# Performance work log

Hardware: AMD Instinct MI355X
Metric: run time of the kernel (lower is better)

Reference implementation:

```python
import jax, jax.numpy as jnp
from jax import lax
import numpy as np

H = 2048
LX = 32
LY = 32


def setup_inputs() -> dict:
    key = jax.random.key(0)
    ks = jax.random.split(key, 9)
    N = LX * LY
    s = 1.0 / np.sqrt(H).astype(np.float32)
    inp = {
        "x": jax.random.normal(ks[0], (N,), jnp.float32),
        # embed: Dense(1 -> H)
        "We": jax.random.normal(ks[1], (1, H), jnp.float32),
        "be": jnp.zeros((H,), jnp.float32),
        # GRUCell input gates (with bias)
        "Wir": jax.random.normal(ks[2], (H, H), jnp.float32) * s,
        "bir": jnp.zeros((H,), jnp.float32),
        "Wiz": jax.random.normal(ks[3], (H, H), jnp.float32) * s,
        "biz": jnp.zeros((H,), jnp.float32),
        "Win": jax.random.normal(ks[4], (H, H), jnp.float32) * s,
        "bin_": jnp.zeros((H,), jnp.float32),
        # GRUCell recurrent gates (hr/hz bias-free, hn with bias, as in flax)
        "Whr": jax.random.normal(ks[5], (H, H), jnp.float32) * s,
        "Whz": jax.random.normal(ks[6], (H, H), jnp.float32) * s,
        "Whn": jax.random.normal(ks[7], (H, H), jnp.float32) * s,
        "bhn": jnp.zeros((H,), jnp.float32),
        "Lx": LX,
        "Ly": LY,
    }
    return inp


def snake_order(Lx: int, Ly: int):
    idx = np.arange(Lx * Ly).reshape(Ly, Lx)
    idx[1::2] = idx[1::2, ::-1]  # reverse odd rows -> snake pattern
    return jnp.asarray(idx.reshape(-1))


def reference(x, We, be, Wir, bir, Wiz, biz, Win, bin_, Whr, Whz, Whn, bhn, Lx, Ly):
    order = snake_order(Lx, Ly)                      # (N,) visit order
    # embed each scalar site value: Dense(1->H), vectorized over all sites
    xe = x[order][:, None] * We[0][None, :] + be     # (N, H)
    # precompute input-gate projections for all steps (same math, batched)
    a_r = xe @ Wir + bir                             # (N, H)
    a_z = xe @ Wiz + biz
    a_n = xe @ Win + bin_
    h0 = jnp.zeros((Whr.shape[0],), xe.dtype)

    def step(h, g):
        ar, az, an = g
        r = jax.nn.sigmoid(ar + h @ Whr)
        z = jax.nn.sigmoid(az + h @ Whz)
        n = jnp.tanh(an + r * (h @ Whn + bhn))
        h_new = (1.0 - z) * n + z * h
        return h_new, None

    h, _ = lax.scan(step, h0, (a_r, a_z, a_n))
    return h
```

## Files before the change

### kernel.cpp

```cpp
#include <hip/hip_runtime.h>

#define HDIM 2048
#define TSTEPS 1024
#define NBLK 256
#define NTHR 512
#define CPB 8
#define TAGM 0x3FFu
#define NREP 8
#define RSTRIDE 2112u

typedef unsigned long long ull;

__device__ __forceinline__ int snake_src(int t) {
    int y = t >> 5, p = t & 31;
    return (y & 1) ? (y * 32 + 31 - p) : t;
}
__device__ __forceinline__ float sigmoid_f(float v) {
    return __builtin_amdgcn_rcpf(1.f + __expf(-v));
}
__device__ __forceinline__ float tanh_f(float v) {
    return 1.f - 2.f * __builtin_amdgcn_rcpf(__expf(2.f * v) + 1.f);
}

__global__ __launch_bounds__(NTHR, 2) void gru_all(
    const float* __restrict__ x,
    const float* __restrict__ We,  const float* __restrict__ be,
    const float* __restrict__ Wir, const float* __restrict__ bir,
    const float* __restrict__ Wiz, const float* __restrict__ biz,
    const float* __restrict__ Win, const float* __restrict__ bin_,
    const float* __restrict__ Whr, const float* __restrict__ Whz,
    const float* __restrict__ Whn, const float* __restrict__ bhn,
    float* __restrict__ out, unsigned* __restrict__ u0, unsigned* __restrict__ u1)
{
    const int tid  = threadIdx.x;
    const int blk  = blockIdx.x;
    const int c    = tid & 7;
    const int r    = tid >> 3;
    const int col  = blk * CPB + c;
    const int row0 = r * 32;
    const int lane = tid & 63, wv = tid >> 6;

    __shared__ __align__(16) float lds_h[2304];
    __shared__ float red[8][6][8];
    __shared__ float sX[TSTEPS];

    for (int i = tid; i < TSTEPS; i += NTHR) sX[i] = x[snake_src(i)];

    float wr[32], wz[32], wn[32];
#pragma unroll
    for (int k = 0; k < 32; ++k) {
        size_t off = (size_t)(row0 + k) * HDIM + col;
        wr[k] = Whr[off];
        wz[k] = Whz[off];
        wn[k] = Whn[off];
    }

    float eR=0,eZ=0,eN=0,bRa=0,bZa=0,bNa=0;
#pragma unroll 8
    for (int k = 0; k < 32; ++k) {
        int row = row0 + k;
        size_t off = (size_t)row * HDIM + col;
        float we = We[row], bb = be[row];
        float w0 = Wir[off], w1 = Wiz[off], w2 = Win[off];
        eR  = fmaf(we, w0, eR);  bRa = fmaf(bb, w0, bRa);
        eZ  = fmaf(we, w1, eZ);  bZa = fmaf(bb, w1, bZa);
        eN  = fmaf(we, w2, eN);  bNa = fmaf(bb, w2, bNa);
    }
#pragma unroll
    for (int m = 8; m < 64; m <<= 1) {
        eR  += __shfl_xor(eR,  m, 64); eZ  += __shfl_xor(eZ,  m, 64);
        eN  += __shfl_xor(eN,  m, 64); bRa += __shfl_xor(bRa, m, 64);
        bZa += __shfl_xor(bZa, m, 64); bNa += __shfl_xor(bNa, m, 64);
    }
    if (lane < 8) {
        red[wv][0][lane]=eR;  red[wv][1][lane]=eZ;  red[wv][2][lane]=eN;
        red[wv][3][lane]=bRa; red[wv][4][lane]=bZa; red[wv][5][lane]=bNa;
    }
    __syncthreads();

    float vrc=0,vzc=0,vnc=0,crc=0,czc=0,cnc=0,bhc=0;
    float aR=0, aZ=0, aN=0;
    unsigned pk1 = 0;
    if (tid < 8) {
#pragma unroll
        for (int w = 0; w < 8; ++w) {
            vrc += red[w][0][tid]; vzc += red[w][1][tid]; vnc += red[w][2][tid];
            crc += red[w][3][tid]; czc += red[w][4][tid]; cnc += red[w][5][tid];
        }
        crc += bir[col]; czc += biz[col]; cnc += bin_[col];
        bhc = bhn[col];

        float x0 = sX[0];
        float ar = fmaf(x0, vrc, crc);
        float az = fmaf(x0, vzc, czc);
        float an = fmaf(x0, vnc, cnc);
        float rg = sigmoid_f(ar), zg = sigmoid_f(az);
        float ng = tanh_f(fmaf(rg, bhc, an));
        float h1 = (1.f - zg) * ng;
        pk1 = ((__float_as_uint(h1) + 512u) & ~TAGM) | 1u;

        float x1 = sX[1];
        aR = fmaf(x1, vrc, crc);
        aZ = fmaf(x1, vzc, czc);
        aN = fmaf(x1, vnc, cnc);
    }
    if (wv == 0) {
        unsigned pkb = __shfl(pk1, lane & 7, 64);
        __hip_atomic_store(&u1[(unsigned)(lane >> 3) * RSTRIDE + (unsigned)blk * 8u + (unsigned)(lane & 7)],
                           pkb, __ATOMIC_RELAXED, __HIP_MEMORY_SCOPE_AGENT);
    }

    const int sbase = tid * 4;
    const int lwb   = sbase + ((sbase >> 6) << 2);
    const int lrb   = row0  + ((row0  >> 6) << 2);
    const int pcol  = col   + ((col   >> 6) << 2);
    const ull  M2   = 0x000003FF000003FFull;
    const size_t repoff = (size_t)(blk & 7) * (RSTRIDE / 2);

    for (int t = 1; t < TSTEPS; ++t) {
        const unsigned* pin  = (t & 1) ? u1 : u0;
        unsigned*       pout = (t & 1) ? u0 : u1;
        const unsigned  tg   = (unsigned)t & TAGM;
        const ull       tg2  = ((ull)tg << 32) | (ull)tg;

        const ull* pp = (const ull*)pin + repoff + 2 * tid;
        ull v0 = __hip_atomic_load(&pp[0], __ATOMIC_RELAXED, __HIP_MEMORY_SCOPE_AGENT);
        ull v1 = __hip_atomic_load(&pp[1], __ATOMIC_RELAXED, __HIP_MEMORY_SCOPE_AGENT);
        while (((v0 ^ tg2) | (v1 ^ tg2)) & M2) {
            __builtin_amdgcn_s_sleep(1);
            v0 = __hip_atomic_load(&pp[0], __ATOMIC_RELAXED, __HIP_MEMORY_SCOPE_AGENT);
            v1 = __hip_atomic_load(&pp[1], __ATOMIC_RELAXED, __HIP_MEMORY_SCOPE_AGENT);
        }
        float4 hq = make_float4(__uint_as_float((unsigned)v0         & ~TAGM),
                                __uint_as_float((unsigned)(v0 >> 32) & ~TAGM),
                                __uint_as_float((unsigned)v1         & ~TAGM),
                                __uint_as_float((unsigned)(v1 >> 32) & ~TAGM));
        *(float4*)&lds_h[lwb] = hq;
        __syncthreads();

        float hold = 0.f;
        if (wv == 0) hold = lds_h[pcol];

        float a0 = 0.f, a1 = 0.f, a2 = 0.f;
#pragma unroll
        for (int k = 0; k < 32; ++k) {
            float hv = lds_h[lrb + k];
            a0 = fmaf(hv, wr[k], a0);
            a1 = fmaf(hv, wz[k], a1);
            a2 = fmaf(hv, wn[k], a2);
        }
#pragma unroll
        for (int m = 8; m < 64; m <<= 1) {
            a0 += __shfl_xor(a0, m, 64);
            a1 += __shfl_xor(a1, m, 64);
            a2 += __shfl_xor(a2, m, 64);
        }
        if (lane < 8) { red[wv][0][lane]=a0; red[wv][1][lane]=a1; red[wv][2][lane]=a2; }
        __syncthreads();

        if (wv == 0) {
            float hnew = 0.f; unsigned pk = 0;
            if (lane < 8) {
                float Sr=0, Sz=0, Sn=0;
#pragma unroll
                for (int w = 0; w < 8; ++w) {
                    Sr += red[w][0][lane]; Sz += red[w][1][lane]; Sn += red[w][2][lane];
                }
                float ar = aR + Sr;
                float az = aZ + Sz;
                float rg = sigmoid_f(ar), zg = sigmoid_f(az);
                float ng = tanh_f(aN + rg * (Sn + bhc));
                hnew = (1.f - zg) * ng + zg * hold;
                pk = ((__float_as_uint(hnew) + 512u) & ~TAGM)
                   | ((unsigned)(t + 1) & TAGM);
            }
            if (t == TSTEPS - 1) {
                if (lane < 8) out[col] = hnew;
            } else {
                unsigned pkb = __shfl(pk, lane & 7, 64);
                __hip_atomic_store(&pout[(unsigned)(lane >> 3) * RSTRIDE + (unsigned)blk * 8u + (unsigned)(lane & 7)],
                                   pkb, __ATOMIC_RELAXED, __HIP_MEMORY_SCOPE_AGENT);
                if (lane < 8) {
                    float xn = sX[t + 1];
                    aR = fmaf(xn, vrc, crc);
                    aZ = fmaf(xn, vzc, czc);
                    aN = fmaf(xn, vnc, cnc);
                }
            }
        }
        __syncthreads();
    }
}

extern "C" void kernel_launch(void* const* d_in, const int* in_sizes, int n_in,
                              void* d_out, int out_size, void* d_ws, size_t ws_size,
                              hipStream_t stream) {
    const float* x    = (const float*)d_in[0];
    const float* We   = (const float*)d_in[1];
    const float* be   = (const float*)d_in[2];
    const float* Wir  = (const float*)d_in[3];
    const float* bir  = (const float*)d_in[4];
    const float* Wiz  = (const float*)d_in[5];
    const float* biz  = (const float*)d_in[6];
    const float* Win  = (const float*)d_in[7];
    const float* bin_ = (const float*)d_in[8];
    const float* Whr  = (const float*)d_in[9];
    const float* Whz  = (const float*)d_in[10];
    const float* Whn  = (const float*)d_in[11];
    const float* bhn  = (const float*)d_in[12];

    unsigned* u0 = (unsigned*)d_ws;
    unsigned* u1 = u0 + NREP * RSTRIDE;

    gru_all<<<NBLK, NTHR, 0, stream>>>(x, We, be, Wir, bir, Wiz, biz, Win, bin_,
                                       Whr, Whz, Whn, bhn,
                                       (float*)d_out, u0, u1);
}
```

Baseline: 2.257 ms.

## Broadcast h via ds_swizzle, LDS atomic reduction, and 16 replicas with 64-bit stores

Each thread now keeps the four h values it polled in registers and shares them within 8-lane groups using ds_swizzle broadcasts. This removes the LDS staging buffer and one __syncthreads per step. The per-wave partial sums are combined with LDS atomicAdd into accumulators pre-seeded with the input-gate terms, replacing the separate reduction array. The h-state is published to 16 replicas using packed 64-bit stores, which spreads polling contention across more copies. Risks are atomicAdd ordering nondeterminism, more global store traffic, and launch_bounds dropping to one block per CU.

Result: slower. 2.468 ms (+9.3%).

```diff
diff --git a/kernel.cpp b/kernel.cpp
--- a/kernel.cpp
+++ b/kernel.cpp
@@ -6,7 +6,7 @@
 #define NTHR 512
 #define CPB 8
 #define TAGM 0x3FFu
-#define NREP 8
+#define NREP 16
 #define RSTRIDE 2112u
 
 typedef unsigned long long ull;
@@ -21,8 +21,13 @@
 __device__ __forceinline__ float tanh_f(float v) {
     return 1.f - 2.f * __builtin_amdgcn_rcpf(__expf(2.f * v) + 1.f);
 }
-
-__global__ __launch_bounds__(NTHR, 2) void gru_all(
+template<int G>
+__device__ __forceinline__ float bcast8(float v) {
+    return __uint_as_float((unsigned)__builtin_amdgcn_ds_swizzle(
+        (int)__float_as_uint(v), (G << 5) | 0x18));
+}
+
+__global__ __launch_bounds__(NTHR, 1) void gru_all(
     const float* __restrict__ x,
     const float* __restrict__ We,  const float* __restrict__ be,
     const float* __restrict__ Wir, const float* __restrict__ bir,
@@ -40,9 +45,10 @@
     const int row0 = r * 32;
     const int lane = tid & 63, wv = tid >> 6;
 
-    __shared__ __align__(16) float lds_h[2304];
     __shared__ float red[8][6][8];
     __shared__ float sX[TSTEPS];
+    __shared__ float sAcc[3][8];
+    __shared__ float sHold[8];
 
     for (int i = tid; i < TSTEPS; i += NTHR) sX[i] = x[snake_src(i)];
 
@@ -79,7 +85,7 @@
     __syncthreads();
 
     float vrc=0,vzc=0,vnc=0,crc=0,czc=0,cnc=0,bhc=0;
-    float aR=0, aZ=0, aN=0;
+    float aN=0;
     unsigned pk1 = 0;
     if (tid < 8) {
 #pragma unroll
@@ -100,22 +106,24 @@
         pk1 = ((__float_as_uint(h1) + 512u) & ~TAGM) | 1u;
 
         float x1 = sX[1];
-        aR = fmaf(x1, vrc, crc);
-        aZ = fmaf(x1, vzc, czc);
-        aN = fmaf(x1, vnc, cnc);
+        sAcc[0][tid] = fmaf(x1, vrc, crc);
+        sAcc[1][tid] = fmaf(x1, vzc, czc);
+        aN           = fmaf(x1, vnc, cnc);
+        sAcc[2][tid] = bhc;
     }
     if (wv == 0) {
-        unsigned pkb = __shfl(pk1, lane & 7, 64);
-        __hip_atomic_store(&u1[(unsigned)(lane >> 3) * RSTRIDE + (unsigned)blk * 8u + (unsigned)(lane & 7)],
-                           pkb, __ATOMIC_RELAXED, __HIP_MEMORY_SCOPE_AGENT);
-    }
-
-    const int sbase = tid * 4;
-    const int lwb   = sbase + ((sbase >> 6) << 2);
-    const int lrb   = row0  + ((row0  >> 6) << 2);
-    const int pcol  = col   + ((col   >> 6) << 2);
-    const ull  M2   = 0x000003FF000003FFull;
-    const size_t repoff = (size_t)(blk & 7) * (RSTRIDE / 2);
+        unsigned c0  = (lane & 3) * 2;
+        unsigned pkA = __shfl(pk1, (int)c0,     64);
+        unsigned pkB = __shfl(pk1, (int)c0 + 1, 64);
+        ull pkk = (ull)pkA | ((ull)pkB << 32);
+        ull* dst = (ull*)u1 + (ull)(lane >> 2) * (RSTRIDE / 2)
+                 + (ull)blk * 4 + (ull)(lane & 3);
+        __hip_atomic_store(dst, pkk, __ATOMIC_RELAXED, __HIP_MEMORY_SCOPE_AGENT);
+    }
+    __syncthreads();
+
+    const ull  M2     = 0x000003FF000003FFull;
+    const ull  repoff = (ull)(blk & 15) * (RSTRIDE / 2);
 
     for (int t = 1; t < TSTEPS; ++t) {
         const unsigned* pin  = (t & 1) ? u1 : u0;
@@ -131,45 +139,49 @@
             v0 = __hip_atomic_load(&pp[0], __ATOMIC_RELAXED, __HIP_MEMORY_SCOPE_AGENT);
             v1 = __hip_atomic_load(&pp[1], __ATOMIC_RELAXED, __HIP_MEMORY_SCOPE_AGENT);
         }
-        float4 hq = make_float4(__uint_as_float((unsigned)v0         & ~TAGM),
-                                __uint_as_float((unsigned)(v0 >> 32) & ~TAGM),
-                                __uint_as_float((unsigned)v1         & ~TAGM),
-                                __uint_as_float((unsigned)(v1 >> 32) & ~TAGM));
-        *(float4*)&lds_h[lwb] = hq;
-        __syncthreads();
-
-        float hold = 0.f;
-        if (wv == 0) hold = lds_h[pcol];
+        float hr0 = __uint_as_float((unsigned)v0         & ~TAGM);
+        float hr1 = __uint_as_float((unsigned)(v0 >> 32) & ~TAGM);
+        float hr2 = __uint_as_float((unsigned)v1         & ~TAGM);
+        float hr3 = __uint_as_float((unsigned)(v1 >> 32) & ~TAGM);
+
+        if ((tid >> 1) == blk) {
+            float* hs = &sHold[(tid & 1) * 4];
+            hs[0] = hr0; hs[1] = hr1; hs[2] = hr2; hs[3] = hr3;
+        }
 
         float a0 = 0.f, a1 = 0.f, a2 = 0.f;
-#pragma unroll
-        for (int k = 0; k < 32; ++k) {
-            float hv = lds_h[lrb + k];
-            a0 = fmaf(hv, wr[k], a0);
-            a1 = fmaf(hv, wz[k], a1);
-            a2 = fmaf(hv, wn[k], a2);
-        }
+#define GRP(G) { \
+        float h0 = bcast8<G>(hr0), h1 = bcast8<G>(hr1); \
+        float h2 = bcast8<G>(hr2), h3 = bcast8<G>(hr3); \
+        a0 = fmaf(h0, wr[4*G+0], a0); a1 = fmaf(h0, wz[4*G+0], a1); a2 = fmaf(h0, wn[4*G+0], a2); \
+        a0 = fmaf(h1, wr[4*G+1], a0); a1 = fmaf(h1, wz[4*G+1], a1); a2 = fmaf(h1, wn[4*G+1], a2); \
+        a0 = fmaf(h2, wr[4*G+2], a0); a1 = fmaf(h2, wz[4*G+2], a1); a2 = fmaf(h2, wn[4*G+2], a2); \
+        a0 = fmaf(h3, wr[4*G+3], a0); a1 = fmaf(h3, wz[4*G+3], a1); a2 = fmaf(h3, wn[4*G+3], a2); }
+        GRP(0) GRP(1) GRP(2) GRP(3) GRP(4) GRP(5) GRP(6) GRP(7)
+#undef GRP
+
 #pragma unroll
         for (int m = 8; m < 64; m <<= 1) {
             a0 += __shfl_xor(a0, m, 64);
             a1 += __shfl_xor(a1, m, 64);
             a2 += __shfl_xor(a2, m, 64);
         }
-        if (lane < 8) { red[wv][0][lane]=a0; red[wv][1][lane]=a1; red[wv][2][lane]=a2; }
+        if (lane < 8) {
+            atomicAdd(&sAcc[0][lane], a0);
+            atomicAdd(&sAcc[1][lane], a1);
+            atomicAdd(&sAcc[2][lane], a2);
+        }
         __syncthreads();
 
         if (wv == 0) {
             float hnew = 0.f; unsigned pk = 0;
             if (lane < 8) {
-                float Sr=0, Sz=0, Sn=0;
-#pragma unroll
-                for (int w = 0; w < 8; ++w) {
-                    Sr += red[w][0][lane]; Sz += red[w][1][lane]; Sn += red[w][2][lane];
-                }
-                float ar = aR + Sr;
-                float az = aZ + Sz;
-                float rg = sigmoid_f(ar), zg = sigmoid_f(az);
-                float ng = tanh_f(aN + rg * (Sn + bhc));
+                float Sr = sAcc[0][lane];
+                float Sz = sAcc[1][lane];
+                float Sn = sAcc[2][lane];
+                float hold = sHold[lane];
+                float rg = sigmoid_f(Sr), zg = sigmoid_f(Sz);
+                float ng = tanh_f(aN + rg * Sn);
                 hnew = (1.f - zg) * ng + zg * hold;
                 pk = ((__float_as_uint(hnew) + 512u) & ~TAGM)
                    | ((unsigned)(t + 1) & TAGM);
@@ -177,14 +189,19 @@
             if (t == TSTEPS - 1) {
                 if (lane < 8) out[col] = hnew;
             } else {
-                unsigned pkb = __shfl(pk, lane & 7, 64);
-                __hip_atomic_store(&pout[(unsigned)(lane >> 3) * RSTRIDE + (unsigned)blk * 8u + (unsigned)(lane & 7)],
-                                   pkb, __ATOMIC_RELAXED, __HIP_MEMORY_SCOPE_AGENT);
+                unsigned c0  = (lane & 3) * 2;
+                unsigned pkA = __shfl(pk, (int)c0,     64);
+                unsigned pkB = __shfl(pk, (int)c0 + 1, 64);
+                ull pkk = (ull)pkA | ((ull)pkB << 32);
+                ull* dst = (ull*)pout + (ull)(lane >> 2) * (RSTRIDE / 2)
+                         + (ull)blk * 4 + (ull)(lane & 3);
+                __hip_atomic_store(dst, pkk, __ATOMIC_RELAXED, __HIP_MEMORY_SCOPE_AGENT);
                 if (lane < 8) {
                     float xn = sX[t + 1];
-                    aR = fmaf(xn, vrc, crc);
-                    aZ = fmaf(xn, vzc, czc);
-                    aN = fmaf(xn, vnc, cnc);
+                    sAcc[0][lane] = fmaf(xn, vrc, crc);
+                    sAcc[1][lane] = fmaf(xn, vzc, czc);
+                    aN            = fmaf(xn, vnc, cnc);
+                    sAcc[2][lane] = bhc;
                 }
             }
         }
```
